# Kernel optimization log

Measured on AMD Instinct MI355X. Metric: run time of the kernel, lower is better.

Reference implementation:

```python
import jax, jax.numpy as jnp
import numpy as np

# Module config (matches init_kwargs)
G, K, S = 64, 3, 2          # base patch size, num scales, scale factor
B, H, W, C = 64, 512, 512, 3
HG, HL = 128, 128
D_IN = K * G * G * C


def setup_inputs() -> dict:
    key = jax.random.key(0)
    kx, kl, k1, k2 = jax.random.split(key, 4)
    x = jax.random.normal(kx, (B, H, W, C), dtype=jnp.float32)
    # glimpse locations in [-1, 1)
    l = jax.random.uniform(kl, (B, 2), minval=-1.0, maxval=1.0, dtype=jnp.float32)
    # fc1: phi (D_IN -> HG); fc2: l (2 -> HL). PyTorch-Linear-like scale.
    W1 = jax.random.normal(k1, (D_IN, HG), dtype=jnp.float32) / np.sqrt(D_IN)
    b1 = jnp.zeros((HG,), dtype=jnp.float32)
    W2 = jax.random.normal(k2, (2, HL), dtype=jnp.float32) / np.sqrt(2.0)
    b2 = jnp.zeros((HL,), dtype=jnp.float32)
    return {"x": x, "l": l, "W1": W1, "b1": b1, "W2": W2, "b2": b2}


def _extract_glimpse(x, l):
    """Retina: k multi-scale patches centered at l, resized to (G,G).
    Returns (B, K, G, G, C)."""
    sizes = [G * S**i for i in range(K)]              # 64, 128, 256
    pad = sizes[-1] // 2 + 1                          # pad once for largest scale
    xp = jnp.pad(x, ((0, 0), (pad, pad), (pad, pad), (0, 0)))
    # denormalize: [-1,1] -> [0,H], truncated to int (torch .long())
    coords = (0.5 * (l + 1.0) * H).astype(jnp.int32)  # (B,2): col0=x, col1=y
    patches = []
    for size in sizes:
        fy = coords[:, 1] - size // 2 + pad
        fx = coords[:, 0] - size // 2 + pad

        def slice_one(img, y0, x0, size=size):
            return jax.lax.dynamic_slice(img, (y0, x0, 0), (size, size, C))

        p = jax.vmap(slice_one)(xp, fy, fx)           # (B, size, size, C)
        f = size // G
        if f > 1:  # downsample by integer factor via average pooling
            p = p.reshape(B, G, f, G, f, C).mean(axis=(2, 4))
        patches.append(p)
    return jnp.stack(patches, axis=1)                 # (B, K, G, G, C)


def reference(x, l, W1, b1, W2, b2):
    phi = _extract_glimpse(x, l).reshape(x.shape[0], -1)   # (B, K*G*G*C)
    phi_out = jax.nn.relu(phi @ W1 + b1)                   # (B, HG)
    l_out = jax.nn.relu(l @ W2 + b2)                       # (B, HL)
    return jax.nn.relu(jnp.concatenate([phi_out, l_out], axis=1))
```

## Files before the change

kernel.cpp:

```cpp
#include <hip/hip_runtime.h>

#define G_     64
#define NK     3
#define NB     64
#define IH     512
#define IW     512
#define NC     3
#define HG_    128
#define HL_    128
#define D_IN_    (NK * G_ * G_ * NC)
#define D_SCALE  (G_ * G_ * NC)
#define KCH      128
#define NCHUNK   (D_IN_ / KCH)
#define BSPLIT   4
#define NBLK     (NCHUNK * BSPLIT)
#define PSTRIDE  (NB * HG_)

template <int F>
__device__ __forceinline__ void scale_body(
    const float* __restrict__ x, const float* __restrict__ l,
    const float* __restrict__ W1, float* __restrict__ P,
    int roff, int d0, int b0, int chunkGlobal,
    float (&phi_s)[16][KCH], float (&red2)[16][HG_], int* cx_s, int* cy_s)
{
    const int tid = threadIdx.x;
    if (tid < 16) {
        float lx = l[(b0 + tid) * 2 + 0];
        float ly = l[(b0 + tid) * 2 + 1];
        cx_s[tid] = (int)((0.5f * (lx + 1.0f)) * 512.0f);
        cy_s[tid] = (int)((0.5f * (ly + 1.0f)) * 512.0f);
    }
    __syncthreads();

    const int dd   = tid & (KCH - 1);
    const int jb0  = (tid >> 7) * 8;
    const int r    = roff + dd;
    const int gy   = r / (G_ * NC);
    const int rem  = r - gy * (G_ * NC);
    const int gx   = rem / NC;
    const int c    = rem - gx * NC;
    constexpr float inv = 1.0f / (float)(F * F);
    constexpr int JU = (F == 4) ? 2 : 8;

#pragma unroll 1
    for (int jo = 0; jo < 8; jo += JU) {
        float sums[JU];
#pragma unroll
        for (int ji = 0; ji < JU; ++ji) {
            const int jb = jb0 + jo + ji;
            const int b  = b0 + jb;
            const int by = cy_s[jb] - 32 * F + gy * F;
            const int bx = cx_s[jb] - 32 * F + gx * F;
            const float* bimg = x + (size_t)b * (IH * IW * NC) + c;
            float s = 0.0f;
#pragma unroll
            for (int dy = 0; dy < F; ++dy) {
                const int y = by + dy;
                const bool yok = (unsigned)y < (unsigned)IH;
#pragma unroll
                for (int dx = 0; dx < F; ++dx) {
                    const int xx = bx + dx;
                    const bool ok = yok && ((unsigned)xx < (unsigned)IW);
                    s += ok ? bimg[(size_t)y * (IW * NC) + xx * NC] : 0.0f;
                }
            }
            sums[ji] = s;
        }
#pragma unroll
        for (int ji = 0; ji < JU; ++ji)
            phi_s[jb0 + jo + ji][dd] = sums[ji] * inv;
    }
    __syncthreads();

    const int hq  = tid & 31;
    const int h0  = hq * 4;
    const int gg  = tid >> 5;
    const int bg4 = (gg & 3) * 4;
    const int dh  = gg >> 2;
    const int db  = dh * 64;

    float4 a0 = {0.f, 0.f, 0.f, 0.f};
    float4 a1 = {0.f, 0.f, 0.f, 0.f};
    float4 a2 = {0.f, 0.f, 0.f, 0.f};
    float4 a3 = {0.f, 0.f, 0.f, 0.f};
    const float* wp = W1 + (size_t)(d0 + db) * HG_ + h0;

#pragma unroll 2
    for (int t = 0; t < 16; ++t) {
        const float4 pv0 = *(const float4*)&phi_s[bg4 + 0][db + 4 * t];
        const float4 pv1 = *(const float4*)&phi_s[bg4 + 1][db + 4 * t];
        const float4 pv2 = *(const float4*)&phi_s[bg4 + 2][db + 4 * t];
        const float4 pv3 = *(const float4*)&phi_s[bg4 + 3][db + 4 * t];
#pragma unroll
        for (int u = 0; u < 4; ++u) {
            const float4 wv = *(const float4*)(wp + (size_t)(4 * t + u) * HG_);
            const float p0 = (&pv0.x)[u];
            const float p1 = (&pv1.x)[u];
            const float p2 = (&pv2.x)[u];
            const float p3 = (&pv3.x)[u];
            a0.x = fmaf(p0, wv.x, a0.x); a0.y = fmaf(p0, wv.y, a0.y);
            a0.z = fmaf(p0, wv.z, a0.z); a0.w = fmaf(p0, wv.w, a0.w);
            a1.x = fmaf(p1, wv.x, a1.x); a1.y = fmaf(p1, wv.y, a1.y);
            a1.z = fmaf(p1, wv.z, a1.z); a1.w = fmaf(p1, wv.w, a1.w);
            a2.x = fmaf(p2, wv.x, a2.x); a2.y = fmaf(p2, wv.y, a2.y);
            a2.z = fmaf(p2, wv.z, a2.z); a2.w = fmaf(p2, wv.w, a2.w);
            a3.x = fmaf(p3, wv.x, a3.x); a3.y = fmaf(p3, wv.y, a3.y);
            a3.z = fmaf(p3, wv.z, a3.z); a3.w = fmaf(p3, wv.w, a3.w);
        }
    }

    if (dh == 1) {
        *(float4*)&red2[bg4 + 0][h0] = a0;
        *(float4*)&red2[bg4 + 1][h0] = a1;
        *(float4*)&red2[bg4 + 2][h0] = a2;
        *(float4*)&red2[bg4 + 3][h0] = a3;
    }
    __syncthreads();
    if (dh == 0) {
        float* pb = P + (size_t)chunkGlobal * PSTRIDE + (size_t)(b0 + bg4) * HG_ + h0;
        const float4 r0 = *(const float4*)&red2[bg4 + 0][h0];
        const float4 r1 = *(const float4*)&red2[bg4 + 1][h0];
        const float4 r2 = *(const float4*)&red2[bg4 + 2][h0];
        const float4 r3 = *(const float4*)&red2[bg4 + 3][h0];
        *(float4*)(pb + 0 * HG_) =
            make_float4(a0.x + r0.x, a0.y + r0.y, a0.z + r0.z, a0.w + r0.w);
        *(float4*)(pb + 1 * HG_) =
            make_float4(a1.x + r1.x, a1.y + r1.y, a1.z + r1.z, a1.w + r1.w);
        *(float4*)(pb + 2 * HG_) =
            make_float4(a2.x + r2.x, a2.y + r2.y, a2.z + r2.z, a2.w + r2.w);
        *(float4*)(pb + 3 * HG_) =
            make_float4(a3.x + r3.x, a3.y + r3.y, a3.z + r3.z, a3.w + r3.w);
    }
}

__global__ __launch_bounds__(256) void fused(
    const float* __restrict__ x, const float* __restrict__ l,
    const float* __restrict__ W1, float* __restrict__ P)
{
    __shared__ float phi_s[16][KCH];
    __shared__ float red2[16][HG_];
    __shared__ int cx_s[16], cy_s[16];

    const int chunkGlobal = blockIdx.x >> 2;
    const int b0 = (blockIdx.x & 3) * 16;
    const int d0 = chunkGlobal * KCH;
    const int chunkLocal = chunkGlobal % 96;
    const int roff = chunkLocal * KCH;

    if (chunkGlobal < 96) {
        scale_body<1>(x, l, W1, P, roff, d0, b0, chunkGlobal, phi_s, red2, cx_s, cy_s);
    } else if (chunkGlobal < 192) {
        scale_body<2>(x, l, W1, P, roff, d0, b0, chunkGlobal, phi_s, red2, cx_s, cy_s);
    } else {
        scale_body<4>(x, l, W1, P, roff, d0, b0, chunkGlobal, phi_s, red2, cx_s, cy_s);
    }
}

__global__ __launch_bounds__(512) void reduce_epilogue(
    const float* __restrict__ P,
    const float* __restrict__ l,
    const float* __restrict__ b1,
    const float* __restrict__ W2,
    const float* __restrict__ b2,
    float* __restrict__ out)
{
    __shared__ float4 red[16][32];
    const int b   = blockIdx.x;
    const int t   = threadIdx.x;
    const int hq  = t & 31;
    const int grp = t >> 5;

    const float4* p4 = (const float4*)P
                     + (size_t)(grp * 18) * (PSTRIDE / 4)
                     + (size_t)b * (HG_ / 4) + hq;
    float sx = 0.f, sy = 0.f, sz = 0.f, sw = 0.f;
#pragma unroll 9
    for (int i = 0; i < 18; ++i) {
        const float4 v = p4[(size_t)i * (PSTRIDE / 4)];
        sx += v.x; sy += v.y; sz += v.z; sw += v.w;
    }
    red[grp][hq] = make_float4(sx, sy, sz, sw);
    __syncthreads();

    if (t < 32) {
        float4 a = red[0][t];
#pragma unroll
        for (int g2 = 1; g2 < 16; ++g2) {
            const float4 v = red[g2][t];
            a.x += v.x; a.y += v.y; a.z += v.z; a.w += v.w;
        }
        const float4 bb = ((const float4*)b1)[t];
        float4 o;
        o.x = fmaxf(a.x + bb.x, 0.0f);
        o.y = fmaxf(a.y + bb.y, 0.0f);
        o.z = fmaxf(a.z + bb.z, 0.0f);
        o.w = fmaxf(a.w + bb.w, 0.0f);
        ((float4*)out)[(size_t)b * ((HG_ + HL_) / 4) + t] = o;
    } else if (t >= 64 && t < 192) {
        const int h = t - 64;
        const float l0 = l[b * 2 + 0];
        const float l1 = l[b * 2 + 1];
        const float v = fmaf(l1, W2[HL_ + h], fmaf(l0, W2[h], b2[h]));
        out[(size_t)b * (HG_ + HL_) + HG_ + h] = fmaxf(v, 0.0f);
    }
}

extern "C" void kernel_launch(void* const* d_in, const int* in_sizes, int n_in,
                              void* d_out, int out_size, void* d_ws, size_t ws_size,
                              hipStream_t stream) {
    const float* x  = (const float*)d_in[0];
    const float* l  = (const float*)d_in[1];
    const float* W1 = (const float*)d_in[2];
    const float* b1 = (const float*)d_in[3];
    const float* W2 = (const float*)d_in[4];
    const float* b2 = (const float*)d_in[5];
    float* out = (float*)d_out;
    float* P = (float*)d_ws;

    fused<<<NBLK, 256, 0, stream>>>(x, l, W1, P);
    reduce_epilogue<<<NB, 512, 0, stream>>>(P, l, b1, W2, b2, out);
}
```

Baseline: 278.2 us.

## Dispatch heaviest scale blocks first and split reduction across more blocks

```diff
diff --git a/kernel.cpp b/kernel.cpp
--- a/kernel.cpp
+++ b/kernel.cpp
@@ -141,22 +141,25 @@
     __shared__ float red2[16][HG_];
     __shared__ int cx_s[16], cy_s[16];
 
-    const int chunkGlobal = blockIdx.x >> 2;
+    const int cg = blockIdx.x >> 2;
     const int b0 = (blockIdx.x & 3) * 16;
-    const int d0 = chunkGlobal * KCH;
-    const int chunkLocal = chunkGlobal % 96;
-    const int roff = chunkLocal * KCH;
-
-    if (chunkGlobal < 96) {
-        scale_body<1>(x, l, W1, P, roff, d0, b0, chunkGlobal, phi_s, red2, cx_s, cy_s);
-    } else if (chunkGlobal < 192) {
-        scale_body<2>(x, l, W1, P, roff, d0, b0, chunkGlobal, phi_s, red2, cx_s, cy_s);
+
+    if (cg < 96) {
+        const int cl = cg;
+        scale_body<4>(x, l, W1, P, cl * KCH, 2 * D_SCALE + cl * KCH, b0, cg,
+                      phi_s, red2, cx_s, cy_s);
+    } else if (cg < 192) {
+        const int cl = cg - 96;
+        scale_body<2>(x, l, W1, P, cl * KCH, D_SCALE + cl * KCH, b0, cg,
+                      phi_s, red2, cx_s, cy_s);
     } else {
-        scale_body<4>(x, l, W1, P, roff, d0, b0, chunkGlobal, phi_s, red2, cx_s, cy_s);
-    }
-}
-
-__global__ __launch_bounds__(512) void reduce_epilogue(
+        const int cl = cg - 192;
+        scale_body<1>(x, l, W1, P, cl * KCH, cl * KCH, b0, cg,
+                      phi_s, red2, cx_s, cy_s);
+    }
+}
+
+__global__ __launch_bounds__(256) void reduce_epilogue(
     const float* __restrict__ P,
     const float* __restrict__ l,
     const float* __restrict__ b1,
@@ -164,40 +167,47 @@
     const float* __restrict__ b2,
     float* __restrict__ out)
 {
-    __shared__ float4 red[16][32];
-    const int b   = blockIdx.x;
-    const int t   = threadIdx.x;
-    const int hq  = t & 31;
-    const int grp = t >> 5;
+    __shared__ float4 red[32][8];
+    const int b    = blockIdx.x >> 2;
+    const int q    = blockIdx.x & 3;
+    const int t    = threadIdx.x;
+    const int lane = t & 7;
+    const int grp  = t >> 3;
 
     const float4* p4 = (const float4*)P
-                     + (size_t)(grp * 18) * (PSTRIDE / 4)
-                     + (size_t)b * (HG_ / 4) + hq;
-    float sx = 0.f, sy = 0.f, sz = 0.f, sw = 0.f;
-#pragma unroll 9
-    for (int i = 0; i < 18; ++i) {
+                     + (size_t)(grp * 9) * (PSTRIDE / 4)
+                     + (size_t)b * (HG_ / 4) + q * 8 + lane;
+    float4 a = make_float4(0.f, 0.f, 0.f, 0.f);
+#pragma unroll
+    for (int i = 0; i < 9; ++i) {
         const float4 v = p4[(size_t)i * (PSTRIDE / 4)];
-        sx += v.x; sy += v.y; sz += v.z; sw += v.w;
-    }
-    red[grp][hq] = make_float4(sx, sy, sz, sw);
-    __syncthreads();
-
-    if (t < 32) {
-        float4 a = red[0][t];
-#pragma unroll
-        for (int g2 = 1; g2 < 16; ++g2) {
-            const float4 v = red[g2][t];
-            a.x += v.x; a.y += v.y; a.z += v.z; a.w += v.w;
+        a.x += v.x; a.y += v.y; a.z += v.z; a.w += v.w;
+    }
+    red[grp][lane] = a;
+    __syncthreads();
+
+#pragma unroll
+    for (int s = 16; s >= 1; s >>= 1) {
+        if (grp < s) {
+            const float4 o = red[grp + s][lane];
+            float4 m = red[grp][lane];
+            m.x += o.x; m.y += o.y; m.z += o.z; m.w += o.w;
+            red[grp][lane] = m;
         }
-        const float4 bb = ((const float4*)b1)[t];
+        __syncthreads();
+    }
+
+    if (t < 8) {
+        const float4 a2 = red[0][t];
+        const float4 bb = ((const float4*)b1)[q * 8 + t];
         float4 o;
-        o.x = fmaxf(a.x + bb.x, 0.0f);
-        o.y = fmaxf(a.y + bb.y, 0.0f);
-        o.z = fmaxf(a.z + bb.z, 0.0f);
-        o.w = fmaxf(a.w + bb.w, 0.0f);
-        ((float4*)out)[(size_t)b * ((HG_ + HL_) / 4) + t] = o;
-    } else if (t >= 64 && t < 192) {
-        const int h = t - 64;
+        o.x = fmaxf(a2.x + bb.x, 0.0f);
+        o.y = fmaxf(a2.y + bb.y, 0.0f);
+        o.z = fmaxf(a2.z + bb.z, 0.0f);
+        o.w = fmaxf(a2.w + bb.w, 0.0f);
+        ((float4*)out)[(size_t)b * ((HG_ + HL_) / 4) + q * 8 + t] = o;
+    } else if (t >= 64 && t < 96) {
+        const int h = q * 32 + (t - 64);
         const float l0 = l[b * 2 + 0];
         const float l1 = l[b * 2 + 1];
         const float v = fmaf(l1, W2[HL_ + h], fmaf(l0, W2[h], b2[h]));
@@ -218,5 +228,5 @@
     float* P = (float*)d_ws;
 
     fused<<<NBLK, 256, 0, stream>>>(x, l, W1, P);
-    reduce_epilogue<<<NB, 512, 0, stream>>>(P, l, b1, W2, b2, out);
-}
+    reduce_epilogue<<<NB * 4, 256, 0, stream>>>(P, l, b1, W2, b2, out);
+}
```

Result: no change. 277.7 us (-0.2%).
